# Optimization experiments

Hardware: AMD Instinct MI355X
Metric: run time of the kernel (lower is better)

Reference implementation:

```python
import jax, jax.numpy as jnp
import numpy as np

# Dimensions (see shape_source): batch, tokens, input dim, attention feature dim, output dim
B, T, D_IN, D_ATTN, D_OUT = 8, 2048, 512, 8, 512
# Weight scale keeps Q,K entries ~N(0, 0.5^2) so scores**power stays finite in fp32
W_SCALE = 0.5 / np.sqrt(D_IN)


def setup_inputs() -> dict:
    key = jax.random.key(0)
    k1, k2, k3, k4 = jax.random.split(key, 4)
    Input = jax.random.normal(k1, (B, T, D_IN), dtype=jnp.float32)
    W_q = jax.random.normal(k2, (D_IN, D_ATTN), dtype=jnp.float32) * W_SCALE
    W_k = jax.random.normal(k3, (D_IN, D_ATTN), dtype=jnp.float32) * W_SCALE
    W_v = jax.random.normal(k4, (D_IN, D_OUT), dtype=jnp.float32) * W_SCALE
    return {"Input": Input, "W_q": W_q, "W_k": W_k, "W_v": W_v, "power": D_ATTN}


def reference(Input, W_q, W_k, W_v, power):
    # QKV projections (torch.mm applied per token)
    Q = jnp.einsum('btd,df->btf', Input, W_q)   # [B,T,D_ATTN]
    K = jnp.einsum('btd,df->btf', Input, W_k)   # [B,T,D_ATTN]
    V = jnp.einsum('btd,do->bto', Input, W_v)   # [B,T,D_OUT]
    # Non-standard score transform: elementwise power by Attention.Feature.Num
    scores = jnp.einsum('btf,bsf->bts', Q, K) ** power  # [B,T,T]
    A = jax.nn.softmax(scores, axis=2)
    # Weighted sum of values
    return jnp.einsum('bts,bso->bto', A, V)  # [B,T,D_OUT]
```

## Files before the change

### kernel.cpp

```cpp
#include <hip/hip_runtime.h>
#include <hip/hip_bf16.h>
#include <stdint.h>


typedef float f32x4_t __attribute__((ext_vector_type(4)));
typedef short s16x8_t __attribute__((ext_vector_type(8)));
typedef unsigned int u32;

static __device__ __forceinline__ unsigned short f2bf(float x){
  union { float f; u32 u; } v; v.f = x;
  return (unsigned short)((v.u + 0x7FFFu + ((v.u >> 16) & 1u)) >> 16);
}

static __device__ __forceinline__ u32 pk2bf(float a, float b){
  __hip_bfloat162 h = __float22bfloat162_rn(float2{a, b});
  union { __hip_bfloat162 h2; u32 u; } c; c.h2 = h;
  return c.u;
}

static __device__ __forceinline__ void gload16(const void* g, void* l){
  __builtin_amdgcn_global_load_lds((const __attribute__((address_space(1))) u32*)g,
                                   (__attribute__((address_space(3))) u32*)l, 16, 0, 0);
}

static __device__ __forceinline__ float dot8(const float* q, const float4& a, const float4& b){
  float s = q[0] * a.x;
  s = fmaf(q[1], a.y, s); s = fmaf(q[2], a.z, s); s = fmaf(q[3], a.w, s);
  s = fmaf(q[4], b.x, s); s = fmaf(q[5], b.y, s); s = fmaf(q[6], b.z, s);
  s = fmaf(q[7], b.w, s);
  return s;
}

__global__ __launch_bounds__(256) void k_prep(const float* __restrict__ Wv,
                                              unsigned short* __restrict__ WvT,
                                              const float* __restrict__ In,
                                              const float* __restrict__ Wq,
                                              const float* __restrict__ Wk,
                                              float* __restrict__ Qo,
                                              float* __restrict__ Ko){
  __shared__ __align__(16) char fs[32768];
  const int t = threadIdx.x;
  if (blockIdx.x < 64){
    float (*tile)[68] = (float(*)[68])fs;
    const int dbase = ((int)blockIdx.x >> 3) * 64;
    const int cbase = ((int)blockIdx.x & 7) * 64;
    {
      const int dl = t >> 2, cq = (t & 3) * 16;
      const float* src = Wv + (size_t)(dbase + dl) * 512 + cbase + cq;
#pragma unroll
      for (int i = 0; i < 16; i += 4){
        float4 v = *(const float4*)(src + i);
        tile[dl][cq + i + 0] = v.x; tile[dl][cq + i + 1] = v.y;
        tile[dl][cq + i + 2] = v.z; tile[dl][cq + i + 3] = v.w;
      }
    }
    __syncthreads();
    const int cl = t >> 2, dq = (t & 3) * 16;
    __align__(16) unsigned short o[16];
#pragma unroll
    for (int i = 0; i < 16; ++i) o[i] = f2bf(tile[dq + i][cl]);
    unsigned short* dst = WvT + (size_t)(cbase + cl) * 512 + dbase + dq;
    *(uint4*)dst = *(const uint4*)o;
    *(uint4*)(dst + 8) = *(const uint4*)(o + 8);
    return;
  }
  float* wt = (float*)fs;
  const int bid = (int)blockIdx.x - 64;
#pragma unroll
  for (int i = 0; i < 16; i += 4){
    float4 vq = *(const float4*)(Wq + t * 16 + i);
    float4 vk = *(const float4*)(Wk + t * 16 + i);
    const float* pq = &vq.x;
    const float* pk = &vk.x;
#pragma unroll
    for (int j = 0; j < 4; ++j){
      int flat = t * 16 + i + j;
      int d = flat >> 3, f = flat & 7;
      wt[f * 512 + ((((d >> 2) ^ f) << 2) | (d & 3))] = pq[j];
      int fk = f + 8;
      wt[fk * 512 + ((((d >> 2) ^ (fk & 7)) << 2) | (d & 3))] = pk[j];
    }
  }
  __syncthreads();
  const int tok = bid * 16 + (t >> 4);
  const int f = t & 15;
  const float* inrow = In + (size_t)tok * 512;
  const float* wrow = &wt[f * 512];
  const int swz = f & 7;
  double acc = 0.0;
  for (int cb = 0; cb < 128; cb += 8){
    float part = 0.f;
#pragma unroll
    for (int c = cb; c < cb + 8; ++c){
      float4 x = *(const float4*)(inrow + c * 4);
      float4 ww = *(const float4*)(wrow + ((c ^ swz) << 2));
      part = fmaf(x.x, ww.x, part); part = fmaf(x.y, ww.y, part);
      part = fmaf(x.z, ww.z, part); part = fmaf(x.w, ww.w, part);
    }
    acc += (double)part;
  }
  float r = (float)acc;
  if (f < 8) Qo[(size_t)tok * 8 + f] = r;
  else       Ko[(size_t)tok * 8 + (f - 8)] = r;
}

__global__ __launch_bounds__(256) void k_vproj(const float* __restrict__ In,
                                               const unsigned short* __restrict__ WvT,
                                               unsigned short* __restrict__ Vg){
  __shared__ __align__(16) char smem[65536];
  char* Ab = smem;
  char* Bb = smem + 16384;
  char* Img = smem + 32768;
  const int t = threadIdx.x;
  const int w = t >> 6, lane = t & 63;
  const int mt = blockIdx.x >> 2, nt = blockIdx.x & 3;
  const int wm = w >> 1, wn = w & 1;
  const int asub = lane & 3;
  int arow[2], acr[2];
#pragma unroll
  for (int i = 0; i < 2; ++i){
    arow[i] = (w * 2 + i) * 16 + (lane >> 2);
    acr[i]  = asub ^ ((arow[i] >> 1) & 3);
  }
  f32x4_t acc[4][4];
#pragma unroll
  for (int m = 0; m < 4; ++m)
#pragma unroll
    for (int n = 0; n < 4; ++n)
      acc[m][n] = (f32x4_t){0.f, 0.f, 0.f, 0.f};

  auto stageB = [&](int kk, int sel){
#pragma unroll
    for (int i = 0; i < 2; ++i){
      int id = w * 2 + i;
      const unsigned short* gb = WvT + (size_t)(nt * 128 + arow[i]) * 512 + kk * 32 + acr[i] * 8;
      gload16(gb, Bb + sel * 8192 + id * 1024);
    }
  };
  auto loadA = [&](int kk, float4* x, float4* y){
#pragma unroll
    for (int i = 0; i < 2; ++i){
      const float* ga = In + (size_t)(mt * 128 + arow[i]) * 512 + kk * 32 + acr[i] * 8;
      x[i] = *(const float4*)ga;
      y[i] = *(const float4*)(ga + 4);
    }
  };
  auto writeA = [&](const float4* x, const float4* y, int sel){
#pragma unroll
    for (int i = 0; i < 2; ++i){
      __align__(16) unsigned short pk[8] = {
        f2bf(x[i].x), f2bf(x[i].y), f2bf(x[i].z), f2bf(x[i].w),
        f2bf(y[i].x), f2bf(y[i].y), f2bf(y[i].z), f2bf(y[i].w)};
      *(uint4*)(Ab + sel * 8192 + arow[i] * 64 + asub * 16) = *(const uint4*)pk;
    }
  };
  {
    float4 x[2], y[2];
    loadA(0, x, y);
    stageB(0, 0);
    writeA(x, y, 0);
    __syncthreads();
  }
  for (int kk = 0; kk < 16; ++kk){
    const int cur = kk & 1;
    float4 x[2], y[2];
    if (kk < 15){
      loadA(kk + 1, x, y);
      stageB(kk + 1, cur ^ 1);
    }
    s16x8_t a[4], bf[4];
#pragma unroll
    for (int m = 0; m < 4; ++m){
      int row = wm * 64 + m * 16 + (lane & 15);
      int chn = (lane >> 4) ^ ((row >> 1) & 3);
      a[m] = *(const s16x8_t*)(Ab + cur * 8192 + row * 64 + chn * 16);
    }
#pragma unroll
    for (int n = 0; n < 4; ++n){
      int col = wn * 64 + n * 16 + (lane & 15);
      int chn = (lane >> 4) ^ ((col >> 1) & 3);
      bf[n] = *(const s16x8_t*)(Bb + cur * 8192 + col * 64 + chn * 16);
    }
#pragma unroll
    for (int m = 0; m < 4; ++m)
#pragma unroll
      for (int n = 0; n < 4; ++n)
        acc[m][n] = __builtin_amdgcn_mfma_f32_16x16x32_bf16(a[m], bf[n], acc[m][n], 0, 0, 0);
    if (kk < 15) writeA(x, y, cur ^ 1);
    __syncthreads();
  }
#pragma unroll
  for (int m = 0; m < 4; ++m){
    const int ktl = wm;
    const int ks2 = m >> 1;
    const int hi = ((m & 1) << 1) | ((lane >> 4) >> 1);
    const int k7b = ((lane >> 4) & 1) * 4;
#pragma unroll
    for (int n = 0; n < 4; ++n){
      const int lo = lane & 15;
      __align__(8) unsigned short pk2[4];
#pragma unroll
      for (int j = 0; j < 4; ++j) pk2[j] = f2bf(acc[m][n][j]);
      int boff = ktl * 16384 + wn * 8192 + n * 2048 + ks2 * 1024 + hi * 256 + lo * 16 + k7b * 2;
      *(uint2*)(Img + boff) = *(const uint2*)pk2;
    }
  }
  __syncthreads();
  const int bq = mt >> 4;
#pragma unroll
  for (int i = 0; i < 8; ++i){
    int G = i * 256 + t;
    int ktl = G >> 10, ghl = (G >> 9) & 1, inner = G & 511;
    unsigned short* dst = Vg + (size_t)bq * 1048576
                        + (size_t)((mt & 15) * 2 + ktl) * 32768
                        + nt * 8192 + ghl * 4096 + inner * 8;
    *(uint4*)dst = *(const uint4*)(Img + G * 16);
  }
}

__global__ __launch_bounds__(512, 4) void k_attn(const float* __restrict__ Qg,
                                                 const float* __restrict__ Kg,
                                                 const unsigned short* __restrict__ Vg,
                                                 float* __restrict__ Out){
  __shared__ __align__(16) char smem[75904];
  const int t = threadIdx.x;
  const int g = t >> 6, lane = t & 63;
  const int row = lane & 31;
  const int dup = lane >> 5;
  const int b = blockIdx.x & 7;
  const int qt = blockIdx.x >> 3;
  const int qbase = qt * 32;

  float qreg[8];
  {
    const float* Qp = Qg + (size_t)(b * 2048 + qbase + row) * 8;
    float4 a = *(const float4*)Qp;
    float4 c = *(const float4*)(Qp + 4);
    qreg[0] = a.x; qreg[1] = a.y; qreg[2] = a.z; qreg[3] = a.w;
    qreg[4] = c.x; qreg[5] = c.y; qreg[6] = c.z; qreg[7] = c.w;
  }
  const float* Kp = Kg + (size_t)b * (2048 * 8);
  const unsigned short* Vb = Vg + (size_t)b * 1048576;
  char* Klds = smem;
  char* Pb = smem + 65536;
  float* red = (float*)(smem + 73728);
  float* fin = (float*)(smem + 75776);

#pragma unroll
  for (int i = 0; i < 8; ++i)
    gload16(Kp + (size_t)(i * 512 + t) * 4, Klds + (i * 512 + t) * 16);
  __syncthreads();

  float amax = 0.f;
  {
    const float* kbase = (const float*)Klds + (g * 8 + dup * 4) * 8;
#pragma unroll 2
    for (int tt = 0; tt < 32; ++tt){
      const float* kb = kbase + tt * 512;
#pragma unroll
      for (int j = 0; j < 4; ++j){
        float4 k0 = *(const float4*)(kb + j * 8);
        float4 k1 = *(const float4*)(kb + j * 8 + 4);
        amax = fmaxf(amax, fabsf(dot8(qreg, k0, k1)));
      }
    }
  }
  red[(g * 2 + dup) * 32 + row] = amax;
  __syncthreads();
  float am = red[row];
#pragma unroll
  for (int s = 1; s < 16; ++s) am = fmaxf(am, red[s * 32 + row]);
  float mreg;
  { float s2 = am * am; float s4 = s2 * s2; mreg = s4 * s4; }
  const float LOG2E = 1.44269504f;
  const float me2 = mreg * LOG2E;
  float lp = 0.f;

  auto score = [&](int tt, int sel){
    const float* kb = (const float*)(Klds) + tt * 512 + (g * 8 + dup * 4) * 8;
    float es[4];
#pragma unroll
    for (int j = 0; j < 4; ++j){
      float4 k0 = *(const float4*)(kb + j * 8);
      float4 k1 = *(const float4*)(kb + j * 8 + 4);
      float s = dot8(qreg, k0, k1);
      float s2 = s * s; float s4 = s2 * s2; float p = s4 * s4;
      es[j] = exp2f(fmaf(p, LOG2E, -me2));
      lp += es[j];
    }
    uint2 pkd; pkd.x = pk2bf(es[0], es[1]); pkd.y = pk2bf(es[2], es[3]);
    *(uint2*)(Pb + sel * 4096 + row * 128 + ((g ^ (row & 7)) << 4) + dup * 8) = pkd;
  };

  f32x4_t acc[2][4];
#pragma unroll
  for (int mm = 0; mm < 2; ++mm)
#pragma unroll
    for (int n = 0; n < 4; ++n)
      acc[mm][n] = (f32x4_t){0.f, 0.f, 0.f, 0.f};

  score(0, 0);
  __syncthreads();

  for (int tt = 0; tt < 32; ++tt){
    const int sel = tt & 1;
    s16x8_t vf[4][2];
    {
      const unsigned short* vb = Vb + (size_t)tt * 32768 + g * 4096 + lane * 8;
#pragma unroll
      for (int n = 0; n < 4; ++n)
#pragma unroll
        for (int ks = 0; ks < 2; ++ks)
          vf[n][ks] = *(const s16x8_t*)(vb + n * 1024 + ks * 512);
    }
    if (tt + 1 < 32) score(tt + 1, sel ^ 1);
    s16x8_t a[2][2];
#pragma unroll
    for (int ks = 0; ks < 2; ++ks)
#pragma unroll
      for (int mm = 0; mm < 2; ++mm){
        int r = mm * 16 + (lane & 15);
        int chn = (ks * 4 + (lane >> 4)) ^ (r & 7);
        a[ks][mm] = *(const s16x8_t*)(Pb + sel * 4096 + r * 128 + (chn << 4));
      }
    __builtin_amdgcn_s_setprio(1);
#pragma unroll
    for (int ks = 0; ks < 2; ++ks)
#pragma unroll
      for (int mm = 0; mm < 2; ++mm)
#pragma unroll
        for (int n = 0; n < 4; ++n)
          acc[mm][n] = __builtin_amdgcn_mfma_f32_16x16x32_bf16(a[ks][mm], vf[n][ks], acc[mm][n], 0, 0, 0);
    __builtin_amdgcn_s_setprio(0);
    __syncthreads();
  }

  red[(g * 2 + dup) * 32 + row] = lp;
  __syncthreads();
  if (t < 32){
    float s = red[t];
#pragma unroll
    for (int s2 = 1; s2 < 16; ++s2) s += red[s2 * 32 + t];
    fin[t] = 1.f / s;
  }
  __syncthreads();

  float* img = (float*)smem;
#pragma unroll
  for (int mm = 0; mm < 2; ++mm){
    float linv[4];
#pragma unroll
    for (int j = 0; j < 4; ++j)
      linv[j] = fin[mm * 16 + ((lane >> 4) << 2) + j];
#pragma unroll
    for (int n = 0; n < 4; ++n){
      int colL = g * 64 + n * 16 + (lane & 15);
#pragma unroll
      for (int j = 0; j < 4; ++j){
        int r16 = ((lane >> 4) << 2) + j;
        img[r16 * 520 + colL] = acc[mm][n][j] * linv[j];
      }
    }
    __syncthreads();
#pragma unroll
    for (int i = 0; i < 4; ++i){
      int idx = i * 512 + t;
      int r16 = idx >> 7, c4 = idx & 127;
      float4 v = *(const float4*)(img + r16 * 520 + c4 * 4);
      *(float4*)(Out + (size_t)(b * 2048 + qbase + mm * 16 + r16) * 512 + c4 * 4) = v;
    }
    __syncthreads();
  }
}

extern "C" void kernel_launch(void* const* d_in, const int* in_sizes, int n_in,
                              void* d_out, int out_size, void* d_ws, size_t ws_size,
                              hipStream_t stream){
  const float* In = (const float*)d_in[0];
  const float* Wq = (const float*)d_in[1];
  const float* Wk = (const float*)d_in[2];
  const float* Wv = (const float*)d_in[3];
  char* ws = (char*)d_ws;
  unsigned short* WvT = (unsigned short*)(ws);
  float* Q            = (float*)(ws + 524288);
  float* K            = (float*)(ws + 1048576);
  unsigned short* Vg  = (unsigned short*)(ws + 1572864);
  float* Out = (float*)d_out;

  hipLaunchKernelGGL(k_prep,  dim3(1088), dim3(256), 0, stream, Wv, WvT, In, Wq, Wk, Q, K);
  hipLaunchKernelGGL(k_vproj, dim3(512),  dim3(256), 0, stream, In, WvT, Vg);
  hipLaunchKernelGGL(k_attn,  dim3(512),  dim3(512), 0, stream, Q, K, Vg, Out);
}
```

Measured before the change: 105.2 us.

## Split Wv transpose out, fuse QK projection with V projection, double-step attention loop

The Wv transpose now runs in its own small kernel, and the Q/K projection blocks are merged into the V-projection kernel so both run concurrently in one launch. The attention loop now handles two key tiles per iteration with four P buffers in LDS, so there is one barrier per two tiles and score computation interleaves with the two MFMA batches. LDS per attention block grows to 81920 bytes, which may reduce occupancy. Register pressure also rises from holding two V fragment sets.

```diff
diff --git a/kernel.cpp b/kernel.cpp
--- a/kernel.cpp
+++ b/kernel.cpp
@@ -31,89 +31,87 @@
   return s;
 }
 
-__global__ __launch_bounds__(256) void k_prep(const float* __restrict__ Wv,
-                                              unsigned short* __restrict__ WvT,
-                                              const float* __restrict__ In,
-                                              const float* __restrict__ Wq,
-                                              const float* __restrict__ Wk,
-                                              float* __restrict__ Qo,
-                                              float* __restrict__ Ko){
-  __shared__ __align__(16) char fs[32768];
+__global__ __launch_bounds__(256) void k_wvT(const float* __restrict__ Wv,
+                                             unsigned short* __restrict__ WvT){
+  __shared__ __align__(16) float tile[64][68];
   const int t = threadIdx.x;
-  if (blockIdx.x < 64){
-    float (*tile)[68] = (float(*)[68])fs;
-    const int dbase = ((int)blockIdx.x >> 3) * 64;
-    const int cbase = ((int)blockIdx.x & 7) * 64;
-    {
-      const int dl = t >> 2, cq = (t & 3) * 16;
-      const float* src = Wv + (size_t)(dbase + dl) * 512 + cbase + cq;
-#pragma unroll
-      for (int i = 0; i < 16; i += 4){
-        float4 v = *(const float4*)(src + i);
-        tile[dl][cq + i + 0] = v.x; tile[dl][cq + i + 1] = v.y;
-        tile[dl][cq + i + 2] = v.z; tile[dl][cq + i + 3] = v.w;
-      }
-    }
-    __syncthreads();
-    const int cl = t >> 2, dq = (t & 3) * 16;
-    __align__(16) unsigned short o[16];
-#pragma unroll
-    for (int i = 0; i < 16; ++i) o[i] = f2bf(tile[dq + i][cl]);
-    unsigned short* dst = WvT + (size_t)(cbase + cl) * 512 + dbase + dq;
-    *(uint4*)dst = *(const uint4*)o;
-    *(uint4*)(dst + 8) = *(const uint4*)(o + 8);
-    return;
-  }
-  float* wt = (float*)fs;
-  const int bid = (int)blockIdx.x - 64;
-#pragma unroll
-  for (int i = 0; i < 16; i += 4){
-    float4 vq = *(const float4*)(Wq + t * 16 + i);
-    float4 vk = *(const float4*)(Wk + t * 16 + i);
-    const float* pq = &vq.x;
-    const float* pk = &vk.x;
-#pragma unroll
-    for (int j = 0; j < 4; ++j){
-      int flat = t * 16 + i + j;
-      int d = flat >> 3, f = flat & 7;
-      wt[f * 512 + ((((d >> 2) ^ f) << 2) | (d & 3))] = pq[j];
-      int fk = f + 8;
-      wt[fk * 512 + ((((d >> 2) ^ (fk & 7)) << 2) | (d & 3))] = pk[j];
-    }
-  }
-  __syncthreads();
-  const int tok = bid * 16 + (t >> 4);
-  const int f = t & 15;
-  const float* inrow = In + (size_t)tok * 512;
-  const float* wrow = &wt[f * 512];
-  const int swz = f & 7;
-  double acc = 0.0;
-  for (int cb = 0; cb < 128; cb += 8){
-    float part = 0.f;
-#pragma unroll
-    for (int c = cb; c < cb + 8; ++c){
-      float4 x = *(const float4*)(inrow + c * 4);
-      float4 ww = *(const float4*)(wrow + ((c ^ swz) << 2));
-      part = fmaf(x.x, ww.x, part); part = fmaf(x.y, ww.y, part);
-      part = fmaf(x.z, ww.z, part); part = fmaf(x.w, ww.w, part);
-    }
-    acc += (double)part;
-  }
-  float r = (float)acc;
-  if (f < 8) Qo[(size_t)tok * 8 + f] = r;
-  else       Ko[(size_t)tok * 8 + (f - 8)] = r;
-}
-
-__global__ __launch_bounds__(256) void k_vproj(const float* __restrict__ In,
+  const int dbase = (blockIdx.x >> 3) * 64;
+  const int cbase = (blockIdx.x & 7) * 64;
+  {
+    const int dl = t >> 2, cq = (t & 3) * 16;
+    const float* src = Wv + (size_t)(dbase + dl) * 512 + cbase + cq;
+#pragma unroll
+    for (int i = 0; i < 16; i += 4){
+      float4 v = *(const float4*)(src + i);
+      tile[dl][cq + i + 0] = v.x; tile[dl][cq + i + 1] = v.y;
+      tile[dl][cq + i + 2] = v.z; tile[dl][cq + i + 3] = v.w;
+    }
+  }
+  __syncthreads();
+  const int cl = t >> 2, dq = (t & 3) * 16;
+  __align__(16) unsigned short o[16];
+#pragma unroll
+  for (int i = 0; i < 16; ++i) o[i] = f2bf(tile[dq + i][cl]);
+  unsigned short* dst = WvT + (size_t)(cbase + cl) * 512 + dbase + dq;
+  *(uint4*)dst = *(const uint4*)o;
+  *(uint4*)(dst + 8) = *(const uint4*)(o + 8);
+}
+
+__global__ __launch_bounds__(256) void k_fused(const float* __restrict__ In,
+                                               const float* __restrict__ Wq,
+                                               const float* __restrict__ Wk,
                                                const unsigned short* __restrict__ WvT,
+                                               float* __restrict__ Qo,
+                                               float* __restrict__ Ko,
                                                unsigned short* __restrict__ Vg){
   __shared__ __align__(16) char smem[65536];
+  const int t = threadIdx.x;
+  if (blockIdx.x < 1024){
+    float* wt = (float*)smem;
+#pragma unroll
+    for (int i = 0; i < 16; i += 4){
+      float4 vq = *(const float4*)(Wq + t * 16 + i);
+      float4 vk = *(const float4*)(Wk + t * 16 + i);
+      const float* pq = &vq.x;
+      const float* pk = &vk.x;
+#pragma unroll
+      for (int j = 0; j < 4; ++j){
+        int flat = t * 16 + i + j;
+        int d = flat >> 3, f = flat & 7;
+        wt[f * 512 + ((((d >> 2) ^ f) << 2) | (d & 3))] = pq[j];
+        int fk = f + 8;
+        wt[fk * 512 + ((((d >> 2) ^ (fk & 7)) << 2) | (d & 3))] = pk[j];
+      }
+    }
+    __syncthreads();
+    const int tok = (int)blockIdx.x * 16 + (t >> 4);
+    const int f = t & 15;
+    const float* inrow = In + (size_t)tok * 512;
+    const float* wrow = &wt[f * 512];
+    const int swz = f & 7;
+    double acc = 0.0;
+    for (int cb = 0; cb < 128; cb += 8){
+      float part = 0.f;
+#pragma unroll
+      for (int c = cb; c < cb + 8; ++c){
+        float4 x = *(const float4*)(inrow + c * 4);
+        float4 ww = *(const float4*)(wrow + ((c ^ swz) << 2));
+        part = fmaf(x.x, ww.x, part); part = fmaf(x.y, ww.y, part);
+        part = fmaf(x.z, ww.z, part); part = fmaf(x.w, ww.w, part);
+      }
+      acc += (double)part;
+    }
+    float r = (float)acc;
+    if (f < 8) Qo[(size_t)tok * 8 + f] = r;
+    else       Ko[(size_t)tok * 8 + (f - 8)] = r;
+    return;
+  }
   char* Ab = smem;
   char* Bb = smem + 16384;
   char* Img = smem + 32768;
-  const int t = threadIdx.x;
+  const int vb = (int)blockIdx.x - 1024;
   const int w = t >> 6, lane = t & 63;
-  const int mt = blockIdx.x >> 2, nt = blockIdx.x & 3;
+  const int mt = vb >> 2, nt = vb & 3;
   const int wm = w >> 1, wn = w & 1;
   const int asub = lane & 3;
   int arow[2], acr[2];
@@ -222,7 +220,7 @@
                                                  const float* __restrict__ Kg,
                                                  const unsigned short* __restrict__ Vg,
                                                  float* __restrict__ Out){
-  __shared__ __align__(16) char smem[75904];
+  __shared__ __align__(16) char smem[81920];
   const int t = threadIdx.x;
   const int g = t >> 6, lane = t & 63;
   const int row = lane & 31;
@@ -243,8 +241,6 @@
   const unsigned short* Vb = Vg + (size_t)b * 1048576;
   char* Klds = smem;
   char* Pb = smem + 65536;
-  float* red = (float*)(smem + 73728);
-  float* fin = (float*)(smem + 75776);
 
 #pragma unroll
   for (int i = 0; i < 8; ++i)
@@ -265,16 +261,18 @@
       }
     }
   }
-  red[(g * 2 + dup) * 32 + row] = amax;
-  __syncthreads();
-  float am = red[row];
-#pragma unroll
-  for (int s = 1; s < 16; ++s) am = fmaxf(am, red[s * 32 + row]);
+  float* prered = (float*)(smem + 65536);
+  prered[(g * 2 + dup) * 32 + row] = amax;
+  __syncthreads();
+  float am = prered[row];
+#pragma unroll
+  for (int s = 1; s < 16; ++s) am = fmaxf(am, prered[s * 32 + row]);
   float mreg;
   { float s2 = am * am; float s4 = s2 * s2; mreg = s4 * s4; }
   const float LOG2E = 1.44269504f;
   const float me2 = mreg * LOG2E;
   float lp = 0.f;
+  __syncthreads();
 
   auto score = [&](int tt, int sel){
     const float* kb = (const float*)(Klds) + tt * 512 + (g * 8 + dup * 4) * 8;
@@ -300,47 +298,83 @@
       acc[mm][n] = (f32x4_t){0.f, 0.f, 0.f, 0.f};
 
   score(0, 0);
-  __syncthreads();
-
-  for (int tt = 0; tt < 32; ++tt){
-    const int sel = tt & 1;
-    s16x8_t vf[4][2];
+  score(1, 1);
+  __syncthreads();
+
+  for (int it = 0; it < 16; ++it){
+    const int half = (it & 1) * 2;
+    const int oh = ((it + 1) & 1) * 2;
+    s16x8_t vfA[4][2];
     {
-      const unsigned short* vb = Vb + (size_t)tt * 32768 + g * 4096 + lane * 8;
+      const unsigned short* vba = Vb + (size_t)(2 * it) * 32768 + g * 4096 + lane * 8;
 #pragma unroll
       for (int n = 0; n < 4; ++n)
 #pragma unroll
         for (int ks = 0; ks < 2; ++ks)
-          vf[n][ks] = *(const s16x8_t*)(vb + n * 1024 + ks * 512);
-    }
-    if (tt + 1 < 32) score(tt + 1, sel ^ 1);
-    s16x8_t a[2][2];
-#pragma unroll
-    for (int ks = 0; ks < 2; ++ks)
-#pragma unroll
-      for (int mm = 0; mm < 2; ++mm){
-        int r = mm * 16 + (lane & 15);
-        int chn = (ks * 4 + (lane >> 4)) ^ (r & 7);
-        a[ks][mm] = *(const s16x8_t*)(Pb + sel * 4096 + r * 128 + (chn << 4));
-      }
-    __builtin_amdgcn_s_setprio(1);
-#pragma unroll
-    for (int ks = 0; ks < 2; ++ks)
-#pragma unroll
-      for (int mm = 0; mm < 2; ++mm)
-#pragma unroll
-        for (int n = 0; n < 4; ++n)
-          acc[mm][n] = __builtin_amdgcn_mfma_f32_16x16x32_bf16(a[ks][mm], vf[n][ks], acc[mm][n], 0, 0, 0);
-    __builtin_amdgcn_s_setprio(0);
-    __syncthreads();
-  }
-
-  red[(g * 2 + dup) * 32 + row] = lp;
+          vfA[n][ks] = *(const s16x8_t*)(vba + n * 1024 + ks * 512);
+    }
+    if (it < 15) score(2 * it + 2, oh);
+    s16x8_t vfB[4][2];
+    {
+      const unsigned short* vbb = Vb + (size_t)(2 * it + 1) * 32768 + g * 4096 + lane * 8;
+#pragma unroll
+      for (int n = 0; n < 4; ++n)
+#pragma unroll
+        for (int ks = 0; ks < 2; ++ks)
+          vfB[n][ks] = *(const s16x8_t*)(vbb + n * 1024 + ks * 512);
+    }
+    {
+      s16x8_t a[2][2];
+#pragma unroll
+      for (int ks = 0; ks < 2; ++ks)
+#pragma unroll
+        for (int mm = 0; mm < 2; ++mm){
+          int r = mm * 16 + (lane & 15);
+          int chn = (ks * 4 + (lane >> 4)) ^ (r & 7);
+          a[ks][mm] = *(const s16x8_t*)(Pb + half * 4096 + r * 128 + (chn << 4));
+        }
+      __builtin_amdgcn_s_setprio(1);
+#pragma unroll
+      for (int ks = 0; ks < 2; ++ks)
+#pragma unroll
+        for (int mm = 0; mm < 2; ++mm)
+#pragma unroll
+          for (int n = 0; n < 4; ++n)
+            acc[mm][n] = __builtin_amdgcn_mfma_f32_16x16x32_bf16(a[ks][mm], vfA[n][ks], acc[mm][n], 0, 0, 0);
+      __builtin_amdgcn_s_setprio(0);
+    }
+    if (it < 15) score(2 * it + 3, oh + 1);
+    {
+      s16x8_t a[2][2];
+#pragma unroll
+      for (int ks = 0; ks < 2; ++ks)
+#pragma unroll
+        for (int mm = 0; mm < 2; ++mm){
+          int r = mm * 16 + (lane & 15);
+          int chn = (ks * 4 + (lane >> 4)) ^ (r & 7);
+          a[ks][mm] = *(const s16x8_t*)(Pb + (half + 1) * 4096 + r * 128 + (chn << 4));
+        }
+      __builtin_amdgcn_s_setprio(1);
+#pragma unroll
+      for (int ks = 0; ks < 2; ++ks)
+#pragma unroll
+        for (int mm = 0; mm < 2; ++mm)
+#pragma unroll
+          for (int n = 0; n < 4; ++n)
+            acc[mm][n] = __builtin_amdgcn_mfma_f32_16x16x32_bf16(a[ks][mm], vfB[n][ks], acc[mm][n], 0, 0, 0);
+      __builtin_amdgcn_s_setprio(0);
+    }
+    __syncthreads();
+  }
+
+  float* postred = (float*)smem;
+  float* fin = (float*)(smem + 65536 + 2048);
+  postred[(g * 2 + dup) * 32 + row] = lp;
   __syncthreads();
   if (t < 32){
-    float s = red[t];
-#pragma unroll
-    for (int s2 = 1; s2 < 16; ++s2) s += red[s2 * 32 + t];
+    float s = postred[t];
+#pragma unroll
+    for (int s2 = 1; s2 < 16; ++s2) s += postred[s2 * 32 + t];
     fin[t] = 1.f / s;
   }
   __syncthreads();
@@ -387,7 +421,7 @@
   unsigned short* Vg  = (unsigned short*)(ws + 1572864);
   float* Out = (float*)d_out;
 
-  hipLaunchKernelGGL(k_prep,  dim3(1088), dim3(256), 0, stream, Wv, WvT, In, Wq, Wk, Q, K);
-  hipLaunchKernelGGL(k_vproj, dim3(512),  dim3(256), 0, stream, In, WvT, Vg);
+  hipLaunchKernelGGL(k_wvT,   dim3(64),   dim3(256), 0, stream, Wv, WvT);
+  hipLaunchKernelGGL(k_fused, dim3(1536), dim3(256), 0, stream, In, Wq, Wk, WvT, Q, K, Vg);
   hipLaunchKernelGGL(k_attn,  dim3(512),  dim3(512), 0, stream, Q, K, Vg, Out);
 }
```

New measurement: 116.1 us. 1.1x slower.
